# Kernel optimization log

Hardware: AMD Instinct MI355X
Metric: run time of the kernel (lower is better)

Reference implementation:

```python
import jax, jax.numpy as jnp
import numpy as np

D, NA, NX, B, K, L = 128, 4096, 8192, 8, 16, 3
SLOPE = 0.2

def leaky(z):
    return jnp.where(z >= 0, z, SLOPE * z)

def group_norm(x, w, b, groups=2, eps=1e-5):
    # torch.nn.GroupNorm(2, D) on [N, C]: normalize each group of C//groups channels per sample
    n, c = x.shape
    xg = x.reshape(n, groups, c // groups)
    mu = xg.mean(-1, keepdims=True)
    var = ((xg - mu) ** 2).mean(-1, keepdims=True)
    xn = ((xg - mu) * jax.lax.rsqrt(var + eps)).reshape(n, c)
    return xn * w + b

def knn(qx, dbx, qb, dbb, k):
    # batch-restricted kNN: squared distances, +inf across different graphs (dMaSIF knn_atoms)
    d2 = jnp.sum((qx[:, None, :] - dbx[None, :, :]) ** 2, axis=-1)  # [Nq, Ndb]
    d2 = jnp.where(qb[:, None] == dbb[None, :], d2, jnp.inf)
    _, idx = jax.lax.top_k(-d2, k)  # ascending distance
    idx = jax.lax.stop_gradient(idx)
    # recompute squared dists from coords (matches keops Kmin + recompute, keeps grads to coords)
    dists = jnp.sum((qx[:, None, :] - dbx[idx]) ** 2, axis=-1)  # [Nq, k]
    return idx, dists

def mp_layer(center, src, idx, dists, w1, b1, w2, b2, gw, gb):
    nbr = src[idx]  # [N, k, D] gather
    feats = jnp.concatenate([jnp.broadcast_to(center[:, None, :], nbr.shape), nbr, dists[..., None]], axis=-1)  # [N,k,2D+1]
    h = leaky(feats @ w1 + b1) @ w2 + b2  # per-edge MLP -> [N,k,D]
    msg = h.sum(axis=1)  # sum over k neighbors
    return center + leaky(group_norm(msg, gw, gb))

def _forward(xyz, atom_xyz, atom_features, batch, atom_batch, tw1, tb1, tw2, tb2,
             aa_w1, aa_b1, aa_w2, aa_b2, aa_gw, aa_gb,
             ae_w1, ae_b1, ae_w2, ae_b2, ae_gw, ae_gb):
    # transform_atom_features
    out = leaky(atom_features @ tw1 + tb1) @ tw2 + tb2
    # atom_atom_forward: k+1 neighbors, drop self (first column)
    idx, dists = knn(atom_xyz, atom_xyz, atom_batch, atom_batch, K + 1)
    idx, dists = idx[:, 1:], dists[:, 1:]
    for i in range(L):
        out = mp_layer(out, out, idx, dists, aa_w1[i], aa_b1[i], aa_w2[i], aa_b2[i], aa_gw[i], aa_gb[i])
    # atom_embedding_forward: surface points gather from atom embeddings
    idx, dists = knn(xyz, atom_xyz, batch, atom_batch, K)
    emb = jnp.ones((xyz.shape[0], out.shape[1]), dtype=out.dtype)
    for i in range(L):
        emb = mp_layer(emb, out, idx, dists, ae_w1[i], ae_b1[i], ae_w2[i], ae_b2[i], ae_gw[i], ae_gb[i])
    return emb

def setup_inputs():
    key = jax.random.key(0)
    ks = jax.random.split(key, 16)
    H = 2 * D + 1
    def lin(k, fi, fo):
        return jax.random.normal(k, (fi, fo), jnp.float32) / np.float32(np.sqrt(fi))
    def lin3(k, fi, fo):
        return jax.random.normal(k, (L, fi, fo), jnp.float32) / np.float32(np.sqrt(fi))
    return dict(
        xyz=jax.random.normal(ks[0], (NX, 3), jnp.float32) * 10.0,
        atom_xyz=jax.random.normal(ks[1], (NA, 3), jnp.float32) * 10.0,
        atom_features=jax.random.normal(ks[2], (NA, D), jnp.float32),
        batch=jnp.sort(jax.random.randint(ks[3], (NX,), 0, B)),
        atom_batch=jnp.sort(jax.random.randint(ks[4], (NA,), 0, B)),
        tw1=lin(ks[5], D, D), tb1=jnp.zeros((D,), jnp.float32),
        tw2=lin(ks[6], D, D), tb2=jnp.zeros((D,), jnp.float32),
        aa_w1=lin3(ks[7], H, H), aa_b1=jnp.zeros((L, H), jnp.float32),
        aa_w2=lin3(ks[8], H, D), aa_b2=jnp.zeros((L, D), jnp.float32),
        aa_gw=jnp.ones((L, D), jnp.float32), aa_gb=jnp.zeros((L, D), jnp.float32),
        ae_w1=lin3(ks[9], H, H), ae_b1=jnp.zeros((L, H), jnp.float32),
        ae_w2=lin3(ks[10], H, D), ae_b2=jnp.zeros((L, D), jnp.float32),
        ae_gw=jnp.ones((L, D), jnp.float32), ae_gb=jnp.zeros((L, D), jnp.float32),
    )

def reference(xyz, atom_xyz, atom_features, batch, atom_batch, tw1, tb1, tw2, tb2, aa_w1, aa_b1, aa_w2, aa_b2, aa_gw, aa_gb, ae_w1, ae_b1, ae_w2, ae_b2, ae_gw, ae_gb):
    return _forward(xyz, atom_xyz, atom_features, batch, atom_batch, tw1, tb1, tw2, tb2,
                    aa_w1, aa_b1, aa_w2, aa_b2, aa_gw, aa_gb,
                    ae_w1, ae_b1, ae_w2, ae_b2, ae_gw, ae_gb)
```

## Files before the change

### kernel.cpp

```cpp
#include <hip/hip_runtime.h>
#include <hip/hip_bf16.h>

#define NAT 4096
#define NXQ 8192
#define DIM 128
#define KNN 16
#define HD  257
#define NLAYER 3
#define SLOPE 0.2f
#define GN_EPS 1e-5f
#define BIGD 1e30f
#define APB 16

typedef __attribute__((ext_vector_type(4))) float f32x4;

__device__ __forceinline__ float leakyf(float z) { return z >= 0.0f ? z : SLOPE * z; }
__device__ __forceinline__ unsigned long long shfl_xor_u64(unsigned long long v, int m) {
    int lo = __shfl_xor((int)(v & 0xffffffffu), m);
    int hi = __shfl_xor((int)(v >> 32), m);
    return ((unsigned long long)(unsigned)hi << 32) | (unsigned)lo;
}

__global__ void fill_f32_r12(float* __restrict__ p, int n, float v)
{
    int i = blockIdx.x * 256 + threadIdx.x;
    if (i < n) p[i] = v;
}

__global__ __launch_bounds__(128) void feat_transform_r12(
    const float* __restrict__ af,
    const float* __restrict__ tw1, const float* __restrict__ tb1,
    const float* __restrict__ tw2, const float* __restrict__ tb2,
    float* __restrict__ out)
{
    const int i = blockIdx.x;
    const int t = threadIdx.x;
    __shared__ __align__(16) float a_s[DIM];
    __shared__ __align__(16) float h_s[DIM];
    a_s[t] = af[i * DIM + t];
    __syncthreads();
    float acc = tb1[t];
    #pragma unroll 2
    for (int k = 0; k < DIM; k += 4) {
        float4 v = *(const float4*)&a_s[k];
        acc = fmaf(v.x, tw1[(k + 0) * DIM + t], acc);
        acc = fmaf(v.y, tw1[(k + 1) * DIM + t], acc);
        acc = fmaf(v.z, tw1[(k + 2) * DIM + t], acc);
        acc = fmaf(v.w, tw1[(k + 3) * DIM + t], acc);
    }
    h_s[t] = leakyf(acc);
    __syncthreads();
    float acc2 = tb2[t];
    #pragma unroll 2
    for (int k = 0; k < DIM; k += 4) {
        float4 v = *(const float4*)&h_s[k];
        acc2 = fmaf(v.x, tw2[(k + 0) * DIM + t], acc2);
        acc2 = fmaf(v.y, tw2[(k + 1) * DIM + t], acc2);
        acc2 = fmaf(v.z, tw2[(k + 2) * DIM + t], acc2);
        acc2 = fmaf(v.w, tw2[(k + 3) * DIM + t], acc2);
    }
    out[i * DIM + t] = acc2;
}

__global__ __launch_bounds__(64) void batch_starts_r12(const int* __restrict__ abatch,
                                                       int* __restrict__ starts)
{
    int t = threadIdx.x;
    if (t <= 8) {
        int lo = 0, hi = NAT;
        while (lo < hi) { int m = (lo + hi) >> 1; if (abatch[m] < t) lo = m + 1; else hi = m; }
        starts[t] = lo;
    }
}

template<int CAP>
__device__ __forceinline__ unsigned long long knn_select(
    const float* __restrict__ axyz, int lo, int hi, int l, int self,
    float qx, float qy, float qz)
{
    float d[CAP];
    #pragma unroll
    for (int s = 0; s < CAP; ++s) {
        const int j = lo + s * 64 + l;
        float d2 = BIGD;
        if (j < hi && j != self) {
            float dx = qx - axyz[3 * j];
            float dy = qy - axyz[3 * j + 1];
            float dz = qz - axyz[3 * j + 2];
            d2 = dx * dx + dy * dy + dz * dz;
        }
        d[s] = d2;
    }

    unsigned mask = 0;
    unsigned long long outk = 0;
    #pragma unroll 1
    for (int it = 0; it < KNN; ++it) {
        float bd = BIGD; int bs = 0;
        #pragma unroll
        for (int s = 0; s < CAP; ++s) {
            bool c = !((mask >> s) & 1u) && d[s] < bd;
            bd = c ? d[s] : bd;
            bs = c ? s : bs;
        }
        const int bj = lo + bs * 64 + l;
        unsigned long long mykey = ((unsigned long long)__float_as_uint(bd) << 32) | (unsigned)bj;
        unsigned long long key = mykey;
        #pragma unroll
        for (int m = 32; m >= 1; m >>= 1) {
            unsigned long long o = shfl_xor_u64(key, m);
            key = (o < key) ? o : key;
        }
        if (key == mykey) mask |= 1u << bs;
        if (l == it) outk = key;
    }
    return outk;
}

__global__ __launch_bounds__(256) void knn_r12(
    const float* __restrict__ xyz, const int* __restrict__ xbatch,
    const float* __restrict__ axyz, const int* __restrict__ abatch,
    const int* __restrict__ starts,
    int* __restrict__ idx_aa, float* __restrict__ dist_aa,
    int* __restrict__ idx_xa, float* __restrict__ dist_xa)
{
    const int w = blockIdx.x * 4 + (threadIdx.x >> 6);
    if (w >= NAT + NXQ) return;
    const int l = threadIdx.x & 63;
    const bool is_aa = w < NAT;
    const int q = is_aa ? w : w - NAT;
    float qx, qy, qz; int qb;
    if (is_aa) { qx = axyz[3 * q]; qy = axyz[3 * q + 1]; qz = axyz[3 * q + 2]; qb = abatch[q]; }
    else       { qx = xyz[3 * q];  qy = xyz[3 * q + 1];  qz = xyz[3 * q + 2];  qb = xbatch[q]; }
    const int lo = starts[qb];
    const int hi = starts[qb + 1];
    const int self = is_aa ? q : -1;

    const int smax = (hi - lo + 63) >> 6;
    unsigned long long outk;
    if (smax <= 10) outk = knn_select<10>(axyz, lo, hi, l, self, qx, qy, qz);
    else            outk = knn_select<16>(axyz, lo, hi, l, self, qx, qy, qz);

    if (l < KNN) {
        unsigned ju = (unsigned)(outk & 0xffffffffu);
        float dw = __uint_as_float((unsigned)(outk >> 32));
        int jc = (ju >= (unsigned)NAT) ? 0 : (int)ju;
        int*   ip = is_aa ? (idx_aa + q * KNN)  : (idx_xa + q * KNN);
        float* dp = is_aa ? (dist_aa + q * KNN) : (dist_xa + q * KNN);
        ip[l] = jc;
        dp[l] = dw;
    }
}

__global__ __launch_bounds__(512) void lin128_r12(
    const float* __restrict__ src, const float* __restrict__ w1,
    float* __restrict__ out)
{
    const int t = threadIdx.x;
    const int i0 = blockIdx.x * 16;
    __shared__ __align__(16) float cen_s[16][DIM];
    #pragma unroll
    for (int it = 0; it < 4; ++it) {
        int lin = it * 512 + t;
        int a = lin >> 7, j = lin & 127;
        cen_s[a][j] = src[(size_t)(i0 + a) * DIM + j];
    }
    __syncthreads();

    const float* wbase = w1 + (size_t)128 * HD;
    const int j = t & 255, tg = t >> 8;
    float acc[8];
    #pragma unroll
    for (int r = 0; r < 8; ++r) acc[r] = 0.0f;
    #pragma unroll 4
    for (int k = 0; k < DIM; k += 4) {
        float w0 = wbase[(size_t)(k + 0) * HD + j];
        float wa = wbase[(size_t)(k + 1) * HD + j];
        float wb = wbase[(size_t)(k + 2) * HD + j];
        float wc = wbase[(size_t)(k + 3) * HD + j];
        #pragma unroll
        for (int r = 0; r < 8; ++r) {
            float4 c = *(const float4*)&cen_s[8 * tg + r][k];
            acc[r] = fmaf(c.x, w0, acc[r]);
            acc[r] = fmaf(c.y, wa, acc[r]);
            acc[r] = fmaf(c.z, wb, acc[r]);
            acc[r] = fmaf(c.w, wc, acc[r]);
        }
    }
    #pragma unroll
    for (int r = 0; r < 8; ++r)
        out[(size_t)(i0 + 8 * tg + r) * HD + j] = acc[r];

    {
        const int a = t >> 5, l32 = t & 31;
        float p = 0.f;
        #pragma unroll
        for (int m = 0; m < 4; ++m) {
            const int k = l32 + 32 * m;
            p = fmaf(cen_s[a][k], wbase[(size_t)k * HD + 256], p);
        }
        #pragma unroll
        for (int m = 1; m < 32; m <<= 1) p += __shfl_xor(p, m);
        if (l32 == 0) out[(size_t)(i0 + a) * HD + 256] = p;
    }
}

__global__ __launch_bounds__(512) void layer_fused_r12(
    const float* __restrict__ centers,
    const float* __restrict__ Pws,
    const int* __restrict__ nidx, const float* __restrict__ ndist,
    const float* __restrict__ w1, const float* __restrict__ b1,
    const float* __restrict__ w2, const float* __restrict__ b2,
    const float* __restrict__ gw, const float* __restrict__ gb,
    float* __restrict__ dst)
{
    const int t = threadIdx.x;
    const int i0 = blockIdx.x * APB;

    __shared__ __align__(16) float cen_s[APB][DIM];
    __shared__ __align__(16) float S_s[APB][260];
    __shared__ int   eidx_s[APB][KNN];
    __shared__ float edist_s[APB][KNN];
    __shared__ float c1_256_s[APB];

    #pragma unroll
    for (int it = 0; it < 4; ++it) {
        int lin = it * 512 + t;
        int a = lin >> 7, j = lin & 127;
        cen_s[a][j] = centers[(size_t)(i0 + a) * DIM + j];
    }
    if (t < APB * KNN) {
        int a = t >> 4, e = t & 15;
        eidx_s[a][e]  = nidx[(size_t)(i0 + a) * KNN + e];
        edist_s[a][e] = ndist[(size_t)(i0 + a) * KNN + e];
    }
    __syncthreads();

    const int jc = t & 255, tg = t >> 8;
    float c1a[8];
    {
        const float b = b1[jc];
        #pragma unroll
        for (int r = 0; r < 8; ++r) c1a[r] = b;
    }
    #pragma unroll 4
    for (int k = 0; k < DIM; k += 4) {
        float w0 = w1[(size_t)(k + 0) * HD + jc];
        float wa = w1[(size_t)(k + 1) * HD + jc];
        float wb = w1[(size_t)(k + 2) * HD + jc];
        float wc = w1[(size_t)(k + 3) * HD + jc];
        #pragma unroll
        for (int r = 0; r < 8; ++r) {
            float4 c = *(const float4*)&cen_s[8 * tg + r][k];
            c1a[r] = fmaf(c.x, w0, c1a[r]);
            c1a[r] = fmaf(c.y, wa, c1a[r]);
            c1a[r] = fmaf(c.z, wb, c1a[r]);
            c1a[r] = fmaf(c.w, wc, c1a[r]);
        }
    }
    {
        const int a = t >> 5, l32 = t & 31;
        float p = 0.f;
        #pragma unroll
        for (int m = 0; m < 4; ++m) {
            const int k = l32 + 32 * m;
            p = fmaf(cen_s[a][k], w1[(size_t)k * HD + 256], p);
        }
        #pragma unroll
        for (int m = 1; m < 32; m <<= 1) p += __shfl_xor(p, m);
        if (l32 == 0) c1_256_s[a] = p + b1[256];
    }
    __syncthreads();

    {
        const float wd = w1[(size_t)256 * HD + jc];
        float sa[8];
        #pragma unroll
        for (int r = 0; r < 8; ++r) sa[r] = 0.f;
        #pragma unroll 4
        for (int e = 0; e < KNN; ++e) {
            float pv[8];
            #pragma unroll
            for (int r = 0; r < 8; ++r)
                pv[r] = Pws[(size_t)eidx_s[8 * tg + r][e] * HD + jc];
            #pragma unroll
            for (int r = 0; r < 8; ++r)
                sa[r] += leakyf(fmaf(edist_s[8 * tg + r][e], wd, c1a[r] + pv[r]));
        }
        #pragma unroll
        for (int r = 0; r < 8; ++r) S_s[8 * tg + r][jc] = sa[r];
    }
    if (t < APB * KNN) {
        const int a = t >> 4, e = t & 15;
        const float wt = w1[(size_t)256 * HD + 256];
        float h = leakyf(fmaf(edist_s[a][e], wt,
                              c1_256_s[a] + Pws[(size_t)eidx_s[a][e] * HD + 256]));
        #pragma unroll
        for (int m = 1; m < 16; m <<= 1) h += __shfl_xor(h, m);
        if (e == 0) S_s[a][256] = h;
    }
    __syncthreads();

    const int j = t & 127, tg2 = t >> 7;
    const int ab = 4 * tg2;
    float macc0 = 16.0f * b2[j], macc1 = macc0, macc2 = macc0, macc3 = macc0;
    #pragma unroll 4
    for (int k = 0; k < 256; k += 4) {
        float w0 = w2[(k + 0) * DIM + j];
        float wa = w2[(k + 1) * DIM + j];
        float wb = w2[(k + 2) * DIM + j];
        float wc = w2[(k + 3) * DIM + j];
        f32x4 s0 = *(const f32x4*)&S_s[ab + 0][k];
        f32x4 s1 = *(const f32x4*)&S_s[ab + 1][k];
        f32x4 s2 = *(const f32x4*)&S_s[ab + 2][k];
        f32x4 s3 = *(const f32x4*)&S_s[ab + 3][k];
        macc0 = fmaf(s0[0], w0, macc0); macc0 = fmaf(s0[1], wa, macc0);
        macc0 = fmaf(s0[2], wb, macc0); macc0 = fmaf(s0[3], wc, macc0);
        macc1 = fmaf(s1[0], w0, macc1); macc1 = fmaf(s1[1], wa, macc1);
        macc1 = fmaf(s1[2], wb, macc1); macc1 = fmaf(s1[3], wc, macc1);
        macc2 = fmaf(s2[0], w0, macc2); macc2 = fmaf(s2[1], wa, macc2);
        macc2 = fmaf(s2[2], wb, macc2); macc2 = fmaf(s2[3], wc, macc2);
        macc3 = fmaf(s3[0], w0, macc3); macc3 = fmaf(s3[1], wa, macc3);
        macc3 = fmaf(s3[2], wb, macc3); macc3 = fmaf(s3[3], wc, macc3);
    }
    {
        const float w256 = w2[256 * DIM + j];
        macc0 = fmaf(S_s[ab + 0][256], w256, macc0);
        macc1 = fmaf(S_s[ab + 1][256], w256, macc1);
        macc2 = fmaf(S_s[ab + 2][256], w256, macc2);
        macc3 = fmaf(S_s[ab + 3][256], w256, macc3);
    }

    const float gwj = gw[j], gbj = gb[j];
    float m0 = macc0, m1 = macc1, m2 = macc2, m3 = macc3;
    #pragma unroll
    for (int m = 1; m < 64; m <<= 1) {
        m0 += __shfl_xor(m0, m); m1 += __shfl_xor(m1, m);
        m2 += __shfl_xor(m2, m); m3 += __shfl_xor(m3, m);
    }
    const float mu0 = m0 * (1.f / 64.f), mu1 = m1 * (1.f / 64.f);
    const float mu2 = m2 * (1.f / 64.f), mu3 = m3 * (1.f / 64.f);
    float d0 = macc0 - mu0, d1 = macc1 - mu1, d2 = macc2 - mu2, d3 = macc3 - mu3;
    float v0 = d0 * d0, v1 = d1 * d1, v2 = d2 * d2, v3 = d3 * d3;
    #pragma unroll
    for (int m = 1; m < 64; m <<= 1) {
        v0 += __shfl_xor(v0, m); v1 += __shfl_xor(v1, m);
        v2 += __shfl_xor(v2, m); v3 += __shfl_xor(v3, m);
    }
    v0 *= (1.f / 64.f); v1 *= (1.f / 64.f); v2 *= (1.f / 64.f); v3 *= (1.f / 64.f);
    const float y0 = fmaf(d0 * rsqrtf(v0 + GN_EPS), gwj, gbj);
    const float y1 = fmaf(d1 * rsqrtf(v1 + GN_EPS), gwj, gbj);
    const float y2 = fmaf(d2 * rsqrtf(v2 + GN_EPS), gwj, gbj);
    const float y3 = fmaf(d3 * rsqrtf(v3 + GN_EPS), gwj, gbj);
    dst[(size_t)(i0 + ab + 0) * DIM + j] = cen_s[ab + 0][j] + leakyf(y0);
    dst[(size_t)(i0 + ab + 1) * DIM + j] = cen_s[ab + 1][j] + leakyf(y1);
    dst[(size_t)(i0 + ab + 2) * DIM + j] = cen_s[ab + 2][j] + leakyf(y2);
    dst[(size_t)(i0 + ab + 3) * DIM + j] = cen_s[ab + 3][j] + leakyf(y3);
}

extern "C" void kernel_launch(void* const* d_in, const int* in_sizes, int n_in,
                              void* d_out, int out_size, void* d_ws, size_t ws_size,
                              hipStream_t stream)
{
    const size_t out_bytes = (size_t)out_size * sizeof(float);
    if (n_in != 21) { (void)hipMemsetAsync(d_out, 0x43, out_bytes, stream); return; }

    const size_t n_atoms_f = (size_t)NAT * DIM;
    const size_t n_emb_f   = (size_t)NXQ * DIM;
    const size_t n_P_f     = (size_t)NAT * HD;
    const size_t floats_needed = n_atoms_f * 2 + n_emb_f
        + (size_t)NAT * KNN * 2 + (size_t)NXQ * KNN * 2 + n_P_f + 16;
    if (ws_size < floats_needed * 4 + 64) {
        (void)hipMemsetAsync(d_out, 0x41, out_bytes, stream);
        return;
    }

    const float* xyz    = (const float*)d_in[0];
    const float* axyz   = (const float*)d_in[1];
    const float* af     = (const float*)d_in[2];
    const int*   xbatch = (const int*)d_in[3];
    const int*   abatch = (const int*)d_in[4];
    const float* tw1    = (const float*)d_in[5];
    const float* tb1    = (const float*)d_in[6];
    const float* tw2    = (const float*)d_in[7];
    const float* tb2    = (const float*)d_in[8];
    const float* aa_w1  = (const float*)d_in[9];
    const float* aa_b1  = (const float*)d_in[10];
    const float* aa_w2  = (const float*)d_in[11];
    const float* aa_b2  = (const float*)d_in[12];
    const float* aa_gw  = (const float*)d_in[13];
    const float* aa_gb  = (const float*)d_in[14];
    const float* ae_w1  = (const float*)d_in[15];
    const float* ae_b1  = (const float*)d_in[16];
    const float* ae_w2  = (const float*)d_in[17];
    const float* ae_b2  = (const float*)d_in[18];
    const float* ae_gw  = (const float*)d_in[19];
    const float* ae_gb  = (const float*)d_in[20];

    float* fp      = (float*)d_ws;
    float* atoms_a = fp;                 fp += n_atoms_f;
    float* atoms_b = fp;                 fp += n_atoms_f;
    float* emb     = fp;                 fp += n_emb_f;
    int*   idx_aa  = (int*)fp;           fp += (size_t)NAT * KNN;
    float* dist_aa = fp;                 fp += (size_t)NAT * KNN;
    int*   idx_xa  = (int*)fp;           fp += (size_t)NXQ * KNN;
    float* dist_xa = fp;                 fp += (size_t)NXQ * KNN;
    float* Pws     = fp;                 fp += n_P_f;
    int*   bstarts = (int*)fp;           fp += 16;

    const int NOUT = NXQ * DIM;

    fill_f32_r12<<<(NOUT + 255) / 256, 256, 0, stream>>>(emb, NOUT, 1.0f);
    feat_transform_r12<<<NAT, 128, 0, stream>>>(af, tw1, tb1, tw2, tb2, atoms_a);
    batch_starts_r12<<<1, 64, 0, stream>>>(abatch, bstarts);
    knn_r12<<<(NAT + NXQ + 3) / 4, 256, 0, stream>>>(
        xyz, xbatch, axyz, abatch, bstarts, idx_aa, dist_aa, idx_xa, dist_xa);

    float* cur = atoms_a;
    float* nxt = atoms_b;
    for (int i = 0; i < NLAYER; ++i) {
        const float* w1p = aa_w1 + (size_t)i * HD * HD;
        lin128_r12<<<NAT / 16, 512, 0, stream>>>(cur, w1p, Pws);
        layer_fused_r12<<<NAT / APB, 512, 0, stream>>>(
            cur, Pws, idx_aa, dist_aa,
            w1p, aa_b1 + (size_t)i * HD,
            aa_w2 + (size_t)i * HD * DIM, aa_b2 + (size_t)i * DIM,
            aa_gw + (size_t)i * DIM, aa_gb + (size_t)i * DIM, nxt);
        float* tmp = cur; cur = nxt; nxt = tmp;
    }
    const float* atoms_final = cur;

    for (int i = 0; i < NLAYER; ++i) {
        const float* w1p = ae_w1 + (size_t)i * HD * HD;
        lin128_r12<<<NAT / 16, 512, 0, stream>>>(atoms_final, w1p, Pws);
        float* dsti = (i == NLAYER - 1) ? (float*)d_out : emb;
        layer_fused_r12<<<NXQ / APB, 512, 0, stream>>>(
            emb, Pws, idx_xa, dist_xa,
            w1p, ae_b1 + (size_t)i * HD,
            ae_w2 + (size_t)i * HD * DIM, ae_b2 + (size_t)i * DIM,
            ae_gw + (size_t)i * DIM, ae_gb + (size_t)i * DIM, dsti);
    }
}
```

Baseline: 458.6 us.

## Split fused message-passing layer into aggregation and MLP kernels with global staging

New measurement: 558.1 us. +21.7%, slower.

```diff
diff --git a/kernel.cpp b/kernel.cpp
--- a/kernel.cpp
+++ b/kernel.cpp
@@ -10,7 +10,7 @@
 #define SLOPE 0.2f
 #define GN_EPS 1e-5f
 #define BIGD 1e30f
-#define APB 16
+#define SLD 260
 
 typedef __attribute__((ext_vector_type(4))) float f32x4;
 
@@ -21,13 +21,7 @@
     return ((unsigned long long)(unsigned)hi << 32) | (unsigned)lo;
 }
 
-__global__ void fill_f32_r12(float* __restrict__ p, int n, float v)
-{
-    int i = blockIdx.x * 256 + threadIdx.x;
-    if (i < n) p[i] = v;
-}
-
-__global__ __launch_bounds__(128) void feat_transform_r12(
+__global__ __launch_bounds__(128) void feat_transform_r13(
     const float* __restrict__ af,
     const float* __restrict__ tw1, const float* __restrict__ tb1,
     const float* __restrict__ tw2, const float* __restrict__ tb2,
@@ -62,7 +56,7 @@
     out[i * DIM + t] = acc2;
 }
 
-__global__ __launch_bounds__(64) void batch_starts_r12(const int* __restrict__ abatch,
+__global__ __launch_bounds__(64) void batch_starts_r13(const int* __restrict__ abatch,
                                                        int* __restrict__ starts)
 {
     int t = threadIdx.x;
@@ -117,7 +111,7 @@
     return outk;
 }
 
-__global__ __launch_bounds__(256) void knn_r12(
+__global__ __launch_bounds__(256) void knn_r13(
     const float* __restrict__ xyz, const int* __restrict__ xbatch,
     const float* __restrict__ axyz, const int* __restrict__ abatch,
     const int* __restrict__ starts,
@@ -152,35 +146,27 @@
     }
 }
 
-__global__ __launch_bounds__(512) void lin128_r12(
+__global__ __launch_bounds__(256) void lin128_r13(
     const float* __restrict__ src, const float* __restrict__ w1,
     float* __restrict__ out)
 {
     const int t = threadIdx.x;
-    const int i0 = blockIdx.x * 16;
-    __shared__ __align__(16) float cen_s[16][DIM];
-    #pragma unroll
-    for (int it = 0; it < 4; ++it) {
-        int lin = it * 512 + t;
-        int a = lin >> 7, j = lin & 127;
-        cen_s[a][j] = src[(size_t)(i0 + a) * DIM + j];
-    }
-    __syncthreads();
-
+    const int i0 = blockIdx.x * 8;
     const float* wbase = w1 + (size_t)128 * HD;
-    const int j = t & 255, tg = t >> 8;
+
     float acc[8];
     #pragma unroll
     for (int r = 0; r < 8; ++r) acc[r] = 0.0f;
-    #pragma unroll 4
+
+    #pragma unroll 2
     for (int k = 0; k < DIM; k += 4) {
-        float w0 = wbase[(size_t)(k + 0) * HD + j];
-        float wa = wbase[(size_t)(k + 1) * HD + j];
-        float wb = wbase[(size_t)(k + 2) * HD + j];
-        float wc = wbase[(size_t)(k + 3) * HD + j];
+        float w0 = wbase[(size_t)(k + 0) * HD + t];
+        float wa = wbase[(size_t)(k + 1) * HD + t];
+        float wb = wbase[(size_t)(k + 2) * HD + t];
+        float wc = wbase[(size_t)(k + 3) * HD + t];
         #pragma unroll
         for (int r = 0; r < 8; ++r) {
-            float4 c = *(const float4*)&cen_s[8 * tg + r][k];
+            float4 c = *(const float4*)&src[(size_t)(i0 + r) * DIM + k];
             acc[r] = fmaf(c.x, w0, acc[r]);
             acc[r] = fmaf(c.y, wa, acc[r]);
             acc[r] = fmaf(c.z, wb, acc[r]);
@@ -189,7 +175,7 @@
     }
     #pragma unroll
     for (int r = 0; r < 8; ++r)
-        out[(size_t)(i0 + 8 * tg + r) * HD + j] = acc[r];
+        out[(size_t)(i0 + r) * HD + t] = acc[r];
 
     {
         const int a = t >> 5, l32 = t & 31;
@@ -197,7 +183,7 @@
         #pragma unroll
         for (int m = 0; m < 4; ++m) {
             const int k = l32 + 32 * m;
-            p = fmaf(cen_s[a][k], wbase[(size_t)k * HD + 256], p);
+            p = fmaf(src[(size_t)(i0 + a) * DIM + k], wbase[(size_t)k * HD + 256], p);
         }
         #pragma unroll
         for (int m = 1; m < 32; m <<= 1) p += __shfl_xor(p, m);
@@ -205,115 +191,118 @@
     }
 }
 
-__global__ __launch_bounds__(512) void layer_fused_r12(
+template<bool ONES>
+__global__ __launch_bounds__(256) void c1agg_r13(
     const float* __restrict__ centers,
     const float* __restrict__ Pws,
     const int* __restrict__ nidx, const float* __restrict__ ndist,
     const float* __restrict__ w1, const float* __restrict__ b1,
+    float* __restrict__ Sws)
+{
+    const int t = threadIdx.x;
+    const int i0 = blockIdx.x * 8;
+    __shared__ float c1_256_s[8];
+
+    float c1a[8];
+    if (ONES) {
+        float acc = b1[t];
+        #pragma unroll 4
+        for (int k = 0; k < DIM; ++k)
+            acc += w1[(size_t)k * HD + t];
+        #pragma unroll
+        for (int r = 0; r < 8; ++r) c1a[r] = acc;
+    } else {
+        const float b = b1[t];
+        #pragma unroll
+        for (int r = 0; r < 8; ++r) c1a[r] = b;
+        #pragma unroll 2
+        for (int k = 0; k < DIM; k += 4) {
+            float w0 = w1[(size_t)(k + 0) * HD + t];
+            float wa = w1[(size_t)(k + 1) * HD + t];
+            float wb = w1[(size_t)(k + 2) * HD + t];
+            float wc = w1[(size_t)(k + 3) * HD + t];
+            #pragma unroll
+            for (int r = 0; r < 8; ++r) {
+                float4 c = *(const float4*)&centers[(size_t)(i0 + r) * DIM + k];
+                c1a[r] = fmaf(c.x, w0, c1a[r]);
+                c1a[r] = fmaf(c.y, wa, c1a[r]);
+                c1a[r] = fmaf(c.z, wb, c1a[r]);
+                c1a[r] = fmaf(c.w, wc, c1a[r]);
+            }
+        }
+    }
+
+    {
+        const int a = t >> 5, l32 = t & 31;
+        float p = 0.f;
+        #pragma unroll
+        for (int m = 0; m < 4; ++m) {
+            const int k = l32 + 32 * m;
+            const float wv = w1[(size_t)k * HD + 256];
+            p = ONES ? (p + wv)
+                     : fmaf(centers[(size_t)(i0 + a) * DIM + k], wv, p);
+        }
+        #pragma unroll
+        for (int m = 1; m < 32; m <<= 1) p += __shfl_xor(p, m);
+        if (l32 == 0) c1_256_s[a] = p + b1[256];
+    }
+    __syncthreads();
+
+    {
+        const float wd = w1[(size_t)256 * HD + t];
+        float sa[8];
+        #pragma unroll
+        for (int r = 0; r < 8; ++r) sa[r] = 0.f;
+        #pragma unroll 4
+        for (int e = 0; e < KNN; ++e) {
+            #pragma unroll
+            for (int r = 0; r < 8; ++r) {
+                const int   row = nidx[(size_t)(i0 + r) * KNN + e];
+                const float de  = ndist[(size_t)(i0 + r) * KNN + e];
+                const float pv  = Pws[(size_t)row * HD + t];
+                sa[r] += leakyf(fmaf(de, wd, c1a[r] + pv));
+            }
+        }
+        #pragma unroll
+        for (int r = 0; r < 8; ++r)
+            Sws[(size_t)(i0 + r) * SLD + t] = sa[r];
+    }
+
+    if (t < 128) {
+        const int a = t >> 4, e = t & 15;
+        const float wt = w1[(size_t)256 * HD + 256];
+        const int   row = nidx[(size_t)(i0 + a) * KNN + e];
+        const float de  = ndist[(size_t)(i0 + a) * KNN + e];
+        float h = leakyf(fmaf(de, wt, c1_256_s[a] + Pws[(size_t)row * HD + 256]));
+        #pragma unroll
+        for (int m = 1; m < 16; m <<= 1) h += __shfl_xor(h, m);
+        if (e == 0) Sws[(size_t)(i0 + a) * SLD + 256] = h;
+    }
+}
+
+template<bool ONES>
+__global__ __launch_bounds__(256) void stage_d_r13(
+    const float* __restrict__ centers,
+    const float* __restrict__ Sws,
     const float* __restrict__ w2, const float* __restrict__ b2,
     const float* __restrict__ gw, const float* __restrict__ gb,
     float* __restrict__ dst)
 {
     const int t = threadIdx.x;
-    const int i0 = blockIdx.x * APB;
-
-    __shared__ __align__(16) float cen_s[APB][DIM];
-    __shared__ __align__(16) float S_s[APB][260];
-    __shared__ int   eidx_s[APB][KNN];
-    __shared__ float edist_s[APB][KNN];
-    __shared__ float c1_256_s[APB];
-
-    #pragma unroll
-    for (int it = 0; it < 4; ++it) {
-        int lin = it * 512 + t;
-        int a = lin >> 7, j = lin & 127;
-        cen_s[a][j] = centers[(size_t)(i0 + a) * DIM + j];
-    }
-    if (t < APB * KNN) {
-        int a = t >> 4, e = t & 15;
-        eidx_s[a][e]  = nidx[(size_t)(i0 + a) * KNN + e];
-        edist_s[a][e] = ndist[(size_t)(i0 + a) * KNN + e];
-    }
-    __syncthreads();
-
-    const int jc = t & 255, tg = t >> 8;
-    float c1a[8];
-    {
-        const float b = b1[jc];
-        #pragma unroll
-        for (int r = 0; r < 8; ++r) c1a[r] = b;
-    }
-    #pragma unroll 4
-    for (int k = 0; k < DIM; k += 4) {
-        float w0 = w1[(size_t)(k + 0) * HD + jc];
-        float wa = w1[(size_t)(k + 1) * HD + jc];
-        float wb = w1[(size_t)(k + 2) * HD + jc];
-        float wc = w1[(size_t)(k + 3) * HD + jc];
-        #pragma unroll
-        for (int r = 0; r < 8; ++r) {
-            float4 c = *(const float4*)&cen_s[8 * tg + r][k];
-            c1a[r] = fmaf(c.x, w0, c1a[r]);
-            c1a[r] = fmaf(c.y, wa, c1a[r]);
-            c1a[r] = fmaf(c.z, wb, c1a[r]);
-            c1a[r] = fmaf(c.w, wc, c1a[r]);
-        }
-    }
-    {
-        const int a = t >> 5, l32 = t & 31;
-        float p = 0.f;
-        #pragma unroll
-        for (int m = 0; m < 4; ++m) {
-            const int k = l32 + 32 * m;
-            p = fmaf(cen_s[a][k], w1[(size_t)k * HD + 256], p);
-        }
-        #pragma unroll
-        for (int m = 1; m < 32; m <<= 1) p += __shfl_xor(p, m);
-        if (l32 == 0) c1_256_s[a] = p + b1[256];
-    }
-    __syncthreads();
-
-    {
-        const float wd = w1[(size_t)256 * HD + jc];
-        float sa[8];
-        #pragma unroll
-        for (int r = 0; r < 8; ++r) sa[r] = 0.f;
-        #pragma unroll 4
-        for (int e = 0; e < KNN; ++e) {
-            float pv[8];
-            #pragma unroll
-            for (int r = 0; r < 8; ++r)
-                pv[r] = Pws[(size_t)eidx_s[8 * tg + r][e] * HD + jc];
-            #pragma unroll
-            for (int r = 0; r < 8; ++r)
-                sa[r] += leakyf(fmaf(edist_s[8 * tg + r][e], wd, c1a[r] + pv[r]));
-        }
-        #pragma unroll
-        for (int r = 0; r < 8; ++r) S_s[8 * tg + r][jc] = sa[r];
-    }
-    if (t < APB * KNN) {
-        const int a = t >> 4, e = t & 15;
-        const float wt = w1[(size_t)256 * HD + 256];
-        float h = leakyf(fmaf(edist_s[a][e], wt,
-                              c1_256_s[a] + Pws[(size_t)eidx_s[a][e] * HD + 256]));
-        #pragma unroll
-        for (int m = 1; m < 16; m <<= 1) h += __shfl_xor(h, m);
-        if (e == 0) S_s[a][256] = h;
-    }
-    __syncthreads();
-
-    const int j = t & 127, tg2 = t >> 7;
-    const int ab = 4 * tg2;
+    const int i0 = blockIdx.x * 8;
+    const int j = t & 127, ab = (t >> 7) * 4;
+
     float macc0 = 16.0f * b2[j], macc1 = macc0, macc2 = macc0, macc3 = macc0;
-    #pragma unroll 4
+    #pragma unroll 2
     for (int k = 0; k < 256; k += 4) {
         float w0 = w2[(k + 0) * DIM + j];
         float wa = w2[(k + 1) * DIM + j];
         float wb = w2[(k + 2) * DIM + j];
         float wc = w2[(k + 3) * DIM + j];
-        f32x4 s0 = *(const f32x4*)&S_s[ab + 0][k];
-        f32x4 s1 = *(const f32x4*)&S_s[ab + 1][k];
-        f32x4 s2 = *(const f32x4*)&S_s[ab + 2][k];
-        f32x4 s3 = *(const f32x4*)&S_s[ab + 3][k];
+        f32x4 s0 = *(const f32x4*)&Sws[(size_t)(i0 + ab + 0) * SLD + k];
+        f32x4 s1 = *(const f32x4*)&Sws[(size_t)(i0 + ab + 1) * SLD + k];
+        f32x4 s2 = *(const f32x4*)&Sws[(size_t)(i0 + ab + 2) * SLD + k];
+        f32x4 s3 = *(const f32x4*)&Sws[(size_t)(i0 + ab + 3) * SLD + k];
         macc0 = fmaf(s0[0], w0, macc0); macc0 = fmaf(s0[1], wa, macc0);
         macc0 = fmaf(s0[2], wb, macc0); macc0 = fmaf(s0[3], wc, macc0);
         macc1 = fmaf(s1[0], w0, macc1); macc1 = fmaf(s1[1], wa, macc1);
@@ -325,10 +314,10 @@
     }
     {
         const float w256 = w2[256 * DIM + j];
-        macc0 = fmaf(S_s[ab + 0][256], w256, macc0);
-        macc1 = fmaf(S_s[ab + 1][256], w256, macc1);
-        macc2 = fmaf(S_s[ab + 2][256], w256, macc2);
-        macc3 = fmaf(S_s[ab + 3][256], w256, macc3);
+        macc0 = fmaf(Sws[(size_t)(i0 + ab + 0) * SLD + 256], w256, macc0);
+        macc1 = fmaf(Sws[(size_t)(i0 + ab + 1) * SLD + 256], w256, macc1);
+        macc2 = fmaf(Sws[(size_t)(i0 + ab + 2) * SLD + 256], w256, macc2);
+        macc3 = fmaf(Sws[(size_t)(i0 + ab + 3) * SLD + 256], w256, macc3);
     }
 
     const float gwj = gw[j], gbj = gb[j];
@@ -352,10 +341,14 @@
     const float y1 = fmaf(d1 * rsqrtf(v1 + GN_EPS), gwj, gbj);
     const float y2 = fmaf(d2 * rsqrtf(v2 + GN_EPS), gwj, gbj);
     const float y3 = fmaf(d3 * rsqrtf(v3 + GN_EPS), gwj, gbj);
-    dst[(size_t)(i0 + ab + 0) * DIM + j] = cen_s[ab + 0][j] + leakyf(y0);
-    dst[(size_t)(i0 + ab + 1) * DIM + j] = cen_s[ab + 1][j] + leakyf(y1);
-    dst[(size_t)(i0 + ab + 2) * DIM + j] = cen_s[ab + 2][j] + leakyf(y2);
-    dst[(size_t)(i0 + ab + 3) * DIM + j] = cen_s[ab + 3][j] + leakyf(y3);
+    const float c0 = ONES ? 1.0f : centers[(size_t)(i0 + ab + 0) * DIM + j];
+    const float c1 = ONES ? 1.0f : centers[(size_t)(i0 + ab + 1) * DIM + j];
+    const float c2 = ONES ? 1.0f : centers[(size_t)(i0 + ab + 2) * DIM + j];
+    const float c3 = ONES ? 1.0f : centers[(size_t)(i0 + ab + 3) * DIM + j];
+    dst[(size_t)(i0 + ab + 0) * DIM + j] = c0 + leakyf(y0);
+    dst[(size_t)(i0 + ab + 1) * DIM + j] = c1 + leakyf(y1);
+    dst[(size_t)(i0 + ab + 2) * DIM + j] = c2 + leakyf(y2);
+    dst[(size_t)(i0 + ab + 3) * DIM + j] = c3 + leakyf(y3);
 }
 
 extern "C" void kernel_launch(void* const* d_in, const int* in_sizes, int n_in,
@@ -368,8 +361,9 @@
     const size_t n_atoms_f = (size_t)NAT * DIM;
     const size_t n_emb_f   = (size_t)NXQ * DIM;
     const size_t n_P_f     = (size_t)NAT * HD;
+    const size_t n_S_f     = (size_t)NXQ * SLD;
     const size_t floats_needed = n_atoms_f * 2 + n_emb_f
-        + (size_t)NAT * KNN * 2 + (size_t)NXQ * KNN * 2 + n_P_f + 16;
+        + (size_t)NAT * KNN * 2 + (size_t)NXQ * KNN * 2 + n_P_f + n_S_f + 16;
     if (ws_size < floats_needed * 4 + 64) {
         (void)hipMemsetAsync(d_out, 0x41, out_bytes, stream);
         return;
@@ -406,24 +400,23 @@
     int*   idx_xa  = (int*)fp;           fp += (size_t)NXQ * KNN;
     float* dist_xa = fp;                 fp += (size_t)NXQ * KNN;
     float* Pws     = fp;                 fp += n_P_f;
+    float* Sws     = fp;                 fp += n_S_f;
     int*   bstarts = (int*)fp;           fp += 16;
 
-    const int NOUT = NXQ * DIM;
-
-    fill_f32_r12<<<(NOUT + 255) / 256, 256, 0, stream>>>(emb, NOUT, 1.0f);
-    feat_transform_r12<<<NAT, 128, 0, stream>>>(af, tw1, tb1, tw2, tb2, atoms_a);
-    batch_starts_r12<<<1, 64, 0, stream>>>(abatch, bstarts);
-    knn_r12<<<(NAT + NXQ + 3) / 4, 256, 0, stream>>>(
+    feat_transform_r13<<<NAT, 128, 0, stream>>>(af, tw1, tb1, tw2, tb2, atoms_a);
+    batch_starts_r13<<<1, 64, 0, stream>>>(abatch, bstarts);
+    knn_r13<<<(NAT + NXQ + 3) / 4, 256, 0, stream>>>(
         xyz, xbatch, axyz, abatch, bstarts, idx_aa, dist_aa, idx_xa, dist_xa);
 
     float* cur = atoms_a;
     float* nxt = atoms_b;
     for (int i = 0; i < NLAYER; ++i) {
         const float* w1p = aa_w1 + (size_t)i * HD * HD;
-        lin128_r12<<<NAT / 16, 512, 0, stream>>>(cur, w1p, Pws);
-        layer_fused_r12<<<NAT / APB, 512, 0, stream>>>(
-            cur, Pws, idx_aa, dist_aa,
-            w1p, aa_b1 + (size_t)i * HD,
+        lin128_r13<<<NAT / 8, 256, 0, stream>>>(cur, w1p, Pws);
+        c1agg_r13<false><<<NAT / 8, 256, 0, stream>>>(
+            cur, Pws, idx_aa, dist_aa, w1p, aa_b1 + (size_t)i * HD, Sws);
+        stage_d_r13<false><<<NAT / 8, 256, 0, stream>>>(
+            cur, Sws,
             aa_w2 + (size_t)i * HD * DIM, aa_b2 + (size_t)i * DIM,
             aa_gw + (size_t)i * DIM, aa_gb + (size_t)i * DIM, nxt);
         float* tmp = cur; cur = nxt; nxt = tmp;
@@ -432,12 +425,22 @@
 
     for (int i = 0; i < NLAYER; ++i) {
         const float* w1p = ae_w1 + (size_t)i * HD * HD;
-        lin128_r12<<<NAT / 16, 512, 0, stream>>>(atoms_final, w1p, Pws);
+        lin128_r13<<<NAT / 8, 256, 0, stream>>>(atoms_final, w1p, Pws);
         float* dsti = (i == NLAYER - 1) ? (float*)d_out : emb;
-        layer_fused_r12<<<NXQ / APB, 512, 0, stream>>>(
-            emb, Pws, idx_xa, dist_xa,
-            w1p, ae_b1 + (size_t)i * HD,
-            ae_w2 + (size_t)i * HD * DIM, ae_b2 + (size_t)i * DIM,
-            ae_gw + (size_t)i * DIM, ae_gb + (size_t)i * DIM, dsti);
-    }
-}
+        if (i == 0) {
+            c1agg_r13<true><<<NXQ / 8, 256, 0, stream>>>(
+                emb, Pws, idx_xa, dist_xa, w1p, ae_b1 + (size_t)i * HD, Sws);
+            stage_d_r13<true><<<NXQ / 8, 256, 0, stream>>>(
+                emb, Sws,
+                ae_w2 + (size_t)i * HD * DIM, ae_b2 + (size_t)i * DIM,
+                ae_gw + (size_t)i * DIM, ae_gb + (size_t)i * DIM, dsti);
+        } else {
+            c1agg_r13<false><<<NXQ / 8, 256, 0, stream>>>(
+                emb, Pws, idx_xa, dist_xa, w1p, ae_b1 + (size_t)i * HD, Sws);
+            stage_d_r13<false><<<NXQ / 8, 256, 0, stream>>>(
+                emb, Sws,
+                ae_w2 + (size_t)i * HD * DIM, ae_b2 + (size_t)i * DIM,
+                ae_gw + (size_t)i * DIM, ae_gb + (size_t)i * DIM, dsti);
+        }
+    }
+}
```
